# Optimization experiments

Measured on AMD Instinct MI355X. Metric: run time of the kernel, lower is better.

## Reference

```python
import jax, jax.numpy as jnp
import numpy as np

B, T = 32, 64
STOCH, DETER, HIDDEN = 1024, 4096, 1024
ACT_DIM, EMBED = 128, 1536
MIN_STD = 0.1
EPS = 1e-3  # dreamerv3-torch uses LayerNorm(eps=1e-3)


def _ln(x, g, b):
    m = jnp.mean(x, -1, keepdims=True)
    v = jnp.var(x, -1, keepdims=True)
    return (x - m) * jax.lax.rsqrt(v + EPS) * g + b


def setup_inputs() -> dict:
    key = jax.random.key(0)
    ks = jax.random.split(key, 24)

    def w(k, fan_in, fan_out):
        return jax.random.normal(k, (fan_in, fan_out), jnp.float32) / np.sqrt(fan_in)

    inp = {
        "embed": jax.random.normal(ks[0], (B, T, EMBED), jnp.float32),
        "action": jax.random.normal(ks[1], (B, T, ACT_DIM), jnp.float32),
        "is_first": jnp.zeros((B, T), jnp.bool_),
        "init_deter": jax.random.normal(ks[2], (B, DETER), jnp.float32),
        "init_stoch": jax.random.normal(ks[3], (B, STOCH), jnp.float32),
        "noise_prior": jax.random.normal(ks[4], (B, T, STOCH), jnp.float32),
        "noise_post": jax.random.normal(ks[5], (B, T, STOCH), jnp.float32),
        # _img_in_layers: Linear(stoch+act -> hidden, no bias) + LN + SiLU
        "W_in": w(ks[6], STOCH + ACT_DIM, HIDDEN),
        "g_in": 1.0 + 0.1 * jax.random.normal(ks[7], (HIDDEN,), jnp.float32),
        "b_in": 0.1 * jax.random.normal(ks[8], (HIDDEN,), jnp.float32),
        # GRUCell: Linear(hidden+deter -> 3*deter, no bias) + LN
        "W_gru": w(ks[9], HIDDEN + DETER, 3 * DETER),
        "g_gru": 1.0 + 0.1 * jax.random.normal(ks[10], (3 * DETER,), jnp.float32),
        "b_gru": 0.1 * jax.random.normal(ks[11], (3 * DETER,), jnp.float32),
        # _img_out_layers: Linear(deter -> hidden, no bias) + LN + SiLU
        "W_imgout": w(ks[12], DETER, HIDDEN),
        "g_io": 1.0 + 0.1 * jax.random.normal(ks[13], (HIDDEN,), jnp.float32),
        "b_io": 0.1 * jax.random.normal(ks[14], (HIDDEN,), jnp.float32),
        # _obs_out_layers: Linear(deter+embed -> hidden, no bias) + LN + SiLU
        "W_obsout": w(ks[15], DETER + EMBED, HIDDEN),
        "g_oo": 1.0 + 0.1 * jax.random.normal(ks[16], (HIDDEN,), jnp.float32),
        "b_oo": 0.1 * jax.random.normal(ks[17], (HIDDEN,), jnp.float32),
        # suff-stats layers: Linear(hidden -> 2*stoch) with bias
        "W_ims": w(ks[18], HIDDEN, 2 * STOCH),
        "b_ims": 0.01 * jax.random.normal(ks[19], (2 * STOCH,), jnp.float32),
        "W_obs": w(ks[20], HIDDEN, 2 * STOCH),
        "b_obs": 0.01 * jax.random.normal(ks[21], (2 * STOCH,), jnp.float32),
    }
    return inp


def _observe(embed, action, init_deter, init_stoch, noise_prior, noise_post,
             W_in, g_in, b_in, W_gru, g_gru, b_gru, W_imgout, g_io, b_io,
             W_obsout, g_oo, b_oo, W_ims, b_ims, W_obs, b_obs):
    def suff_stats(h, W, b, noise):
        stats = h @ W + b
        mean, std = jnp.split(stats, 2, -1)
        std = jax.nn.softplus(std) + MIN_STD  # std_act='softplus', mean_act='none'
        return mean, std, mean + std * noise

    def step(carry, xs):
        deter, stoch = carry
        e, a, n_p, n_q = xs
        # img_in: concat(prev_stoch, action) -> Linear -> LN -> SiLU
        x = jax.nn.silu(_ln(jnp.concatenate([stoch, a], -1) @ W_in, g_in, b_in))
        # GRUCell with layernorm (update_bias = -1)
        parts = _ln(jnp.concatenate([x, deter], -1) @ W_gru, g_gru, b_gru)
        reset, cand, update = jnp.split(parts, 3, -1)
        reset = jax.nn.sigmoid(reset)
        cand = jnp.tanh(reset * cand)
        update = jax.nn.sigmoid(update - 1.0)
        deter = update * cand + (1.0 - update) * deter
        # prior (imagination) suff stats + sample
        h_p = jax.nn.silu(_ln(deter @ W_imgout, g_io, b_io))
        mean_p, std_p, stoch_p = suff_stats(h_p, W_ims, b_ims, n_p)
        # posterior (observation) suff stats + sample
        h_q = jax.nn.silu(_ln(jnp.concatenate([deter, e], -1) @ W_obsout, g_oo, b_oo))
        mean_q, std_q, stoch_q = suff_stats(h_q, W_obs, b_obs, n_q)
        out = jnp.concatenate([deter, stoch_q, mean_q, std_q, stoch_p, mean_p, std_p], -1)
        return (deter, stoch_q), out

    xs = (jnp.swapaxes(embed, 0, 1), jnp.swapaxes(action, 0, 1),
          jnp.swapaxes(noise_prior, 0, 1), jnp.swapaxes(noise_post, 0, 1))
    _, outs = jax.lax.scan(step, (init_deter, init_stoch), xs)
    return jnp.swapaxes(outs, 0, 1)  # [B, T, deter + 6*stoch]


def reference(embed, action, is_first, init_deter, init_stoch, noise_prior, noise_post,
              W_in, g_in, b_in, W_gru, g_gru, b_gru, W_imgout, g_io, b_io,
              W_obsout, g_oo, b_oo, W_ims, b_ims, W_obs, b_obs):
    # is_first is all-False and state is given, so the init-mixing branch is never taken
    del is_first
    return _observe(embed, action, init_deter, init_stoch, noise_prior, noise_post,
                    W_in, g_in, b_in, W_gru, g_gru, b_gru, W_imgout, g_io, b_io,
                    W_obsout, g_oo, b_oo, W_ims, b_ims, W_obs, b_obs)
```

## Files before the change

### kernel.cpp

```cpp
#include <hip/hip_runtime.h>
#include <hip/hip_bf16.h>

#define T_ 64
#define DETER_ 4096
#define GRUN 12288

typedef __attribute__((ext_vector_type(8))) __bf16 bf16x8;
typedef __attribute__((ext_vector_type(4))) float f32x4;
typedef __attribute__((ext_vector_type(8))) unsigned short u16x8;
typedef __attribute__((ext_vector_type(4))) unsigned short u16x4;

__device__ inline unsigned short f2bf(float f) {
    union { float f; unsigned u; } x; x.f = f;
    unsigned r = x.u + 0x7fffu + ((x.u >> 16) & 1u);
    return (unsigned short)(r >> 16);
}
__device__ inline float sigmoidf_(float v) { return 1.f / (1.f + __expf(-v)); }
__device__ inline float siluf_(float v)    { return v / (1.f + __expf(-v)); }
__device__ inline float softplusf_(float v){ return fmaxf(v, 0.f) + __logf(1.f + __expf(-fabsf(v))); }
__device__ inline float tanhf_(float v)    { return 2.f / (1.f + __expf(-2.f * v)) - 1.f; }

__device__ inline void barrier_() {
    asm volatile("" ::: "memory");
    __builtin_amdgcn_s_barrier();
    asm volatile("" ::: "memory");
}
template <int N> __device__ inline void vmwaitN() {
    asm volatile("s_waitcnt vmcnt(%0)" :: "i"(N) : "memory");
}
__device__ inline void lgkmwait_() {
    asm volatile("s_waitcnt lgkmcnt(0)" ::: "memory");
}


__global__ __launch_bounds__(256) void k_pack(const float* __restrict__ W,
                                              unsigned short* __restrict__ dst,
                                              int K, int N) {
    long fid = (long)blockIdx.x * 256 + threadIdx.x;
    long nfr = (long)K * N / 8;
    if (fid >= nfr) return;
    int lane = (int)(fid & 63);
    long tile = fid >> 6;
    int ktiles = K >> 5;
    int k_t = (int)(tile % ktiles);
    int n_t = (int)(tile / ktiles);
    int c = lane & 15, kb = lane >> 4;
    int k0 = k_t * 32 + kb * 8;
    int n = n_t * 16 + c;
    unsigned short v[8];
#pragma unroll
    for (int i = 0; i < 8; i++) v[i] = f2bf(W[(long)(k0 + i) * N + n]);
    *reinterpret_cast<u16x8*>(dst + fid * 8) = *reinterpret_cast<u16x8*>(v);
}

__global__ __launch_bounds__(256) void k_conv(const float* __restrict__ s,
                                              unsigned short* __restrict__ d, long n) {
    long i = ((long)blockIdx.x * 256 + threadIdx.x) * 4;
    if (i >= n) return;
    f32x4 v = *reinterpret_cast<const f32x4*>(s + i);
    unsigned short o[4];
#pragma unroll
    for (int k = 0; k < 4; k++) o[k] = f2bf(v[k]);
    *reinterpret_cast<u16x4*>(d + i) = *reinterpret_cast<u16x4*>(o);
}

__global__ __launch_bounds__(256) void k_copy(const float* __restrict__ s,
                                              float* __restrict__ d, long n) {
    long i = ((long)blockIdx.x * 256 + threadIdx.x) * 4;
    if (i >= n) return;
    *reinterpret_cast<f32x4*>(d + i) = *reinterpret_cast<const f32x4*>(s + i);
}


template <int CW>
__device__ inline void stage_glds(unsigned short* chunk, const unsigned short* __restrict__ src,
                                  long ld, long k0) {
    constexpr int NI = (32 * CW * 2) / 4096;
    int wv = (int)threadIdx.x >> 6, lane = (int)threadIdx.x & 63;
#pragma unroll
    for (int i = 0; i < NI; ++i) {
        int obase = (wv * NI + i) << 10;
        int o = obase + lane * 16;
        int row = o / (CW * 2);
        int cb = o - row * (CW * 2);
        int gb = cb ^ ((row & 7) << 4);
        const char* ga = (const char*)(src + (long)row * ld + k0) + gb;
        __builtin_amdgcn_global_load_lds(
            (const __attribute__((address_space(1))) void*)ga,
            (__attribute__((address_space(3))) void*)(chunk + (obase >> 1)),
            16, 0, 0);
    }
}

__device__ inline void stage_ln512(unsigned short* chunk, const float* __restrict__ raw,
                                   int ld, int col0,
                                   const float* __restrict__ g, const float* __restrict__ b,
                                   const float* s_mean, const float* s_rstd) {
    int tid = threadIdx.x;
#pragma unroll
    for (int i = 0; i < 8; ++i) {
        int e = tid * 8 + i * 2048;
        int row = e >> 9, col = e & 511;
        float m = s_mean[row], rs = s_rstd[row];
        const float* sp = raw + (long)row * ld + col0 + col;
        unsigned short pk[8];
#pragma unroll
        for (int j = 0; j < 8; ++j) {
            float ln = (sp[j] - m) * rs * g[col0 + col + j] + b[col0 + col + j];
            pk[j] = f2bf(siluf_(ln));
        }
        int dcol = col ^ ((row & 7) << 3);
        *reinterpret_cast<u16x8*>(chunk + row * 512 + dcol) = *reinterpret_cast<u16x8*>(pk);
    }
}

__device__ inline void stage_ln256(unsigned short* chunk, const float* __restrict__ raw,
                                   int ld, int col0,
                                   const float* __restrict__ g, const float* __restrict__ b,
                                   const float* s_mean, const float* s_rstd) {
    int tid = threadIdx.x;
#pragma unroll
    for (int i = 0; i < 4; ++i) {
        int e = tid * 8 + i * 2048;
        int row = e >> 8, col = e & 255;
        float m = s_mean[row], rs = s_rstd[row];
        const float* sp = raw + (long)row * ld + col0 + col;
        unsigned short pk[8];
#pragma unroll
        for (int j = 0; j < 8; ++j) {
            float ln = (sp[j] - m) * rs * g[col0 + col + j] + b[col0 + col + j];
            pk[j] = f2bf(siluf_(ln));
        }
        int dcol = col ^ ((row & 7) << 3);
        *reinterpret_cast<u16x8*>(chunk + row * 256 + dcol) = *reinterpret_cast<u16x8*>(pk);
    }
}

__device__ inline void stage_lnsum(unsigned short* chunk, const float* __restrict__ hpart,
                                   const float* __restrict__ eprep, int t, int col0,
                                   const float* __restrict__ g, const float* __restrict__ b,
                                   const float* s_mean, const float* s_rstd) {
    int tid = threadIdx.x;
#pragma unroll
    for (int i = 0; i < 8; ++i) {
        int e = tid * 8 + i * 2048;
        int row = e >> 9, col = e & 511;
        int k = col0 + col;
        float m = s_mean[row], rs = s_rstd[row];
        const float* h0 = hpart + (long)row * 1024 + k;
        const float* ep = eprep + ((long)row * T_ + t) * 1024 + k;
        unsigned short pk[8];
#pragma unroll
        for (int jj = 0; jj < 8; jj += 4) {
            f32x4 v = *reinterpret_cast<const f32x4*>(h0 + jj);
            v += *reinterpret_cast<const f32x4*>(h0 + 32768 + jj);
            v += *reinterpret_cast<const f32x4*>(h0 + 65536 + jj);
            v += *reinterpret_cast<const f32x4*>(h0 + 98304 + jj);
            v += *reinterpret_cast<const f32x4*>(ep + jj);
#pragma unroll
            for (int j2 = 0; j2 < 4; ++j2) {
                float ln = (v[j2] - m) * rs * g[k + jj + j2] + b[k + jj + j2];
                pk[jj + j2] = f2bf(siluf_(ln));
            }
        }
        int dcol = col ^ ((row & 7) << 3);
        *reinterpret_cast<u16x8*>(chunk + row * 512 + dcol) = *reinterpret_cast<u16x8*>(pk);
    }
}

template <int CW>
__device__ inline void mfma_rh(const unsigned short* chunk, int row, int kb,
                               const unsigned short* __restrict__ bp, f32x4& acc) {
    constexpr int NKT = CW / 32;
    const unsigned short* ap = chunk + row * CW;
    int sw = (row & 7) << 3;
#pragma unroll
    for (int kt = 0; kt < NKT; ++kt) {
        bf16x8 a = *reinterpret_cast<const bf16x8*>(ap + ((kb * 8 + kt * 32) ^ sw));
        bf16x8 b = *reinterpret_cast<const bf16x8*>(bp + (long)kt * 512);
        acc = __builtin_amdgcn_mfma_f32_16x16x32_bf16(a, b, acc, 0, 0, 0);
    }
}

template <int CW>
__device__ inline void mfma2(const unsigned short* chunk, int c, int kb,
                             const unsigned short* __restrict__ bp,
                             f32x4& acc0, f32x4& acc1) {
    constexpr int NKT = CW / 32;
    const unsigned short* ap0 = chunk + c * CW;
    const unsigned short* ap1 = chunk + (16 + c) * CW;
    int sw = (c & 7) << 3;
#pragma unroll
    for (int kt = 0; kt < NKT; ++kt) {
        int off = (kb * 8 + kt * 32) ^ sw;
        bf16x8 b = *reinterpret_cast<const bf16x8*>(bp + (long)kt * 512);
        bf16x8 a0 = *reinterpret_cast<const bf16x8*>(ap0 + off);
        bf16x8 a1 = *reinterpret_cast<const bf16x8*>(ap1 + off);
        acc0 = __builtin_amdgcn_mfma_f32_16x16x32_bf16(a0, b, acc0, 0, 0, 0);
        acc1 = __builtin_amdgcn_mfma_f32_16x16x32_bf16(a1, b, acc1, 0, 0, 0);
    }
}

template <int CW, int NG, int NL>
__global__ __launch_bounds__(256) void k_gemm32(
    const unsigned short* __restrict__ Bp, int Ktiles, int ktg0,
    const unsigned short* __restrict__ srcA, long ldA,
    const float* __restrict__ lnraw, int lnld,
    const float* __restrict__ g_ln, const float* __restrict__ b_ln,
    const float* __restrict__ pstats, int nslab_in,
    const float* __restrict__ addin, long addin_ld,
    float* __restrict__ outp, long out_ld,
    float* __restrict__ partials, long prows)
{
    constexpr int NCH = NG + NL;
    constexpr int NI = (32 * CW * 2) / 4096;
    __shared__ __align__(16) unsigned short sb[2][32 * CW];
    __shared__ float s_out[32][34];
    __shared__ float s_mean[32], s_rstd[32];
    int tid = threadIdx.x;
    if (NL > 0) {
        if (tid < 32) {
            float s = 0.f, q = 0.f;
            for (int j = 0; j < nslab_in; ++j) {
                s += pstats[((long)j * 32 + tid) * 2];
                q += pstats[((long)j * 32 + tid) * 2 + 1];
            }
            float m = s * (1.f / 1024.f);
            s_mean[tid] = m;
            s_rstd[tid] = rsqrtf(q * (1.f / 1024.f) - m * m + 1e-3f);
        }
        __syncthreads();
    }
    int rowbase = blockIdx.y * 32;
    const unsigned short* srcAr = srcA + (long)rowbase * ldA;
    int lane = tid & 63, wv = tid >> 6;
    int nt = wv >> 1, rh = wv & 1;
    int c = lane & 15, kb = lane >> 4;
    int mrow = rh * 16 + c;
    long ntg = (long)blockIdx.x * 2 + nt;
    const unsigned short* bbase = Bp + (long)ntg * Ktiles * 512 + lane * 8;
    f32x4 acc = {0.f, 0.f, 0.f, 0.f};
    stage_glds<CW>(sb[0], srcAr, ldA, 0);
    for (int ch = 0; ch < NCH; ++ch) {
        int nx = ch + 1;
        if (nx < NG) stage_glds<CW>(sb[nx & 1], srcAr, ldA, (long)nx * CW);
        else if (nx < NCH) stage_ln512(sb[nx & 1], lnraw, lnld, (nx - NG) * 512,
                                       g_ln, b_ln, s_mean, s_rstd);
        if (ch < NG) { if (nx < NG) vmwaitN<NI>(); else vmwaitN<0>(); }
        if (nx >= NG && nx < NCH) lgkmwait_();
        barrier_();
        int kt0 = (ch < NG) ? (ktg0 + ch * (CW / 32)) : ((ch - NG) * 16);
        mfma_rh<CW>(sb[ch & 1], mrow, kb, bbase + (long)kt0 * 512, acc);
        barrier_();
    }
    __syncthreads();
#pragma unroll
    for (int j = 0; j < 4; ++j) s_out[rh * 16 + kb * 4 + j][nt * 16 + c] = acc[j];
    __syncthreads();
    int orow = tid >> 3, c4 = (tid & 7) * 4;
    long rg = rowbase + orow;
    float v[4]; float s = 0.f, q = 0.f;
#pragma unroll
    for (int i = 0; i < 4; ++i) {
        float x = s_out[orow][c4 + i];
        if (addin) x += addin[rg * addin_ld + blockIdx.x * 32 + c4 + i];
        v[i] = x; s += x; q += x * x;
    }
#pragma unroll
    for (int i = 0; i < 4; ++i) outp[rg * out_ld + blockIdx.x * 32 + c4 + i] = v[i];
    if (partials) {
#pragma unroll
        for (int m = 1; m < 8; m <<= 1) { s += __shfl_xor(s, m); q += __shfl_xor(q, m); }
        if ((tid & 7) == 0) {
            partials[((long)blockIdx.x * prows + rg) * 2] = s;
            partials[((long)blockIdx.x * prows + rg) * 2 + 1] = q;
        }
    }
}

__global__ __launch_bounds__(256, 3) void k_gru4(
    const unsigned short* __restrict__ Bp,
    const unsigned short* __restrict__ deterb,
    const float* __restrict__ x_raw, const float* __restrict__ px,
    const float* __restrict__ g_in, const float* __restrict__ b_in,
    float* __restrict__ Gp)
{
    __shared__ __align__(16) unsigned short sb[2][32 * 256];
    __shared__ float s_out[32][66];
    __shared__ float s_mean[32], s_rstd[32];
    int tid = threadIdx.x, lane = tid & 63, wv = tid >> 6;
    int c = lane & 15, kb = lane >> 4;
    int kq = blockIdx.y;
    long ntg = (long)blockIdx.x * 4 + wv;
    const unsigned short* bb = Bp + ntg * 160 * 512 + lane * 8;
    f32x4 acc0 = {0, 0, 0, 0}, acc1 = {0, 0, 0, 0};

    if (kq == 0) {
        if (tid < 32) {
            float s = 0.f, q = 0.f;
            for (int j = 0; j < 32; ++j) {
                s += px[((long)j * 32 + tid) * 2];
                q += px[((long)j * 32 + tid) * 2 + 1];
            }
            float m = s * (1.f / 1024.f);
            s_mean[tid] = m;
            s_rstd[tid] = rsqrtf(q * (1.f / 1024.f) - m * m + 1e-3f);
        }
        __syncthreads();
        stage_glds<256>(sb[0], deterb, 4096, 0);
        stage_ln256(sb[1], x_raw, 1024, 0, g_in, b_in, s_mean, s_rstd);
        vmwaitN<0>(); barrier_();
        mfma2<256>(sb[0], c, kb, bb + (long)32 * 512, acc0, acc1);
        barrier_();
        stage_ln256(sb[0], x_raw, 1024, 256, g_in, b_in, s_mean, s_rstd);
        lgkmwait_(); barrier_();
        mfma2<256>(sb[1], c, kb, bb, acc0, acc1);
        barrier_();
        stage_ln256(sb[1], x_raw, 1024, 512, g_in, b_in, s_mean, s_rstd);
        lgkmwait_(); barrier_();
        mfma2<256>(sb[0], c, kb, bb + (long)8 * 512, acc0, acc1);
        barrier_();
        stage_ln256(sb[0], x_raw, 1024, 768, g_in, b_in, s_mean, s_rstd);
        lgkmwait_(); barrier_();
        mfma2<256>(sb[1], c, kb, bb + (long)16 * 512, acc0, acc1);
        barrier_();
        mfma2<256>(sb[0], c, kb, bb + (long)24 * 512, acc0, acc1);
    } else {
        long o0 = 256 + (long)(kq - 1) * 1280;
        int kt0 = 40 + (kq - 1) * 40;
        stage_glds<256>(sb[0], deterb, 4096, o0);
        stage_glds<256>(sb[1], deterb, 4096, o0 + 256);
        for (int ch = 0; ch < 5; ++ch) {
            if (ch < 4) vmwaitN<4>(); else vmwaitN<0>();
            barrier_();
            mfma2<256>(sb[ch & 1], c, kb, bb + (long)(kt0 + 8 * ch) * 512, acc0, acc1);
            barrier_();
            if (ch + 2 < 5)
                stage_glds<256>(sb[ch & 1], deterb, 4096, o0 + 256 * (ch + 2));
        }
    }
    __syncthreads();
#pragma unroll
    for (int j = 0; j < 4; ++j) {
        s_out[kb * 4 + j][wv * 16 + c] = acc0[j];
        s_out[16 + kb * 4 + j][wv * 16 + c] = acc1[j];
    }
    __syncthreads();
    int row = tid >> 3, c8 = (tid & 7) * 8;
    float* G = Gp + (long)kq * 32 * GRUN + (long)row * GRUN + blockIdx.x * 64 + c8;
#pragma unroll
    for (int i = 0; i < 8; ++i) G[i] = s_out[row][c8 + i];
}

__global__ __launch_bounds__(1024) void k_deter4(
    const float* __restrict__ Gp,
    const float* __restrict__ g_gru, const float* __restrict__ b_gru,
    float* __restrict__ deterf, unsigned short* __restrict__ deterb,
    unsigned short* __restrict__ deter_allb, float* __restrict__ out, int t)
{
    __shared__ float gsh[GRUN];
    __shared__ float red[32];
    int r = blockIdx.x, tid = threadIdx.x;
    int lane = tid & 63, wv = tid >> 6;
    const float* g0 = Gp + (long)r * GRUN;
    float s = 0.f, q = 0.f;
#pragma unroll
    for (int i = 0; i < 3; ++i) {
        int col = (tid + i * 1024) * 4;
        f32x4 v = *reinterpret_cast<const f32x4*>(g0 + col);
        v += *reinterpret_cast<const f32x4*>(g0 + 393216 + col);
        v += *reinterpret_cast<const f32x4*>(g0 + 786432 + col);
        v += *reinterpret_cast<const f32x4*>(g0 + 1179648 + col);
        *reinterpret_cast<f32x4*>(gsh + col) = v;
#pragma unroll
        for (int j = 0; j < 4; ++j) { s += v[j]; q += v[j] * v[j]; }
    }
#pragma unroll
    for (int m = 1; m < 64; m <<= 1) { s += __shfl_xor(s, m); q += __shfl_xor(q, m); }
    if (lane == 0) { red[wv] = s; red[16 + wv] = q; }
    __syncthreads();
    float fs = 0.f, fq = 0.f;
#pragma unroll
    for (int i = 0; i < 16; ++i) { fs += red[i]; fq += red[16 + i]; }
    float mean = fs * (1.f / 12288.f);
    float rstd = rsqrtf(fq * (1.f / 12288.f) - mean * mean + 1e-3f);
    long orow = (long)r * T_ + t;
#pragma unroll
    for (int it = 0; it < 2; ++it) {
        int j = tid * 2 + it * 2048;
        float2 rr = *reinterpret_cast<const float2*>(gsh + j);
        float2 cc = *reinterpret_cast<const float2*>(gsh + 4096 + j);
        float2 uu = *reinterpret_cast<const float2*>(gsh + 8192 + j);
        float2 dd = *reinterpret_cast<const float2*>(deterf + (long)r * DETER_ + j);
        float dn[2]; unsigned short db[2];
#pragma unroll
        for (int i = 0; i < 2; ++i) {
            float gv = (i == 0) ? rr.x : rr.y;
            float cv = (i == 0) ? cc.x : cc.y;
            float uv = (i == 0) ? uu.x : uu.y;
            float dv = (i == 0) ? dd.x : dd.y;
            float lr = (gv - mean) * rstd * g_gru[j + i] + b_gru[j + i];
            float lc = (cv - mean) * rstd * g_gru[4096 + j + i] + b_gru[4096 + j + i];
            float lu = (uv - mean) * rstd * g_gru[8192 + j + i] + b_gru[8192 + j + i];
            float reset = sigmoidf_(lr);
            float cand = tanhf_(reset * lc);
            float upd = sigmoidf_(lu - 1.f);
            dn[i] = upd * cand + (1.f - upd) * dv;
            db[i] = f2bf(dn[i]);
        }
        float2 nd; nd.x = dn[0]; nd.y = dn[1];
        *reinterpret_cast<float2*>(deterf + (long)r * DETER_ + j) = nd;
        unsigned pk = (unsigned)db[0] | ((unsigned)db[1] << 16);
        *reinterpret_cast<unsigned*>(deterb + (long)r * DETER_ + j) = pk;
        *reinterpret_cast<unsigned*>(deter_allb + orow * DETER_ + j) = pk;
        *reinterpret_cast<float2*>(out + orow * 10240 + j) = nd;
    }
}

__global__ __launch_bounds__(256) void k_h4(
    const unsigned short* __restrict__ Wood,
    const unsigned short* __restrict__ deterb,
    float* __restrict__ hpart)
{
    __shared__ __align__(16) unsigned short sb[2][32 * 512];
    __shared__ float s_out[32][66];
    int tid = threadIdx.x, lane = tid & 63, wv = tid >> 6;
    int c = lane & 15, kb = lane >> 4;
    int n = blockIdx.x, kq = blockIdx.y;
    const unsigned short* bbase = Wood + ((long)(n * 4 + wv) * 128) * 512 + lane * 8;
    f32x4 acc0 = {0,0,0,0}, acc1 = {0,0,0,0};
    stage_glds<512>(sb[0], deterb, 4096, (long)kq * 1024);
    stage_glds<512>(sb[1], deterb, 4096, (long)kq * 1024 + 512);
    vmwaitN<8>(); barrier_();
    mfma2<512>(sb[0], c, kb, bbase + (long)(kq * 32) * 512, acc0, acc1);
    vmwaitN<0>(); barrier_();
    mfma2<512>(sb[1], c, kb, bbase + (long)(kq * 32 + 16) * 512, acc0, acc1);
    __syncthreads();
#pragma unroll
    for (int j = 0; j < 4; ++j) {
        s_out[kb * 4 + j][wv * 16 + c] = acc0[j];
        s_out[16 + kb * 4 + j][wv * 16 + c] = acc1[j];
    }
    __syncthreads();
    int row = tid >> 3, c8 = (tid & 7) * 8;
    float* hp = hpart + (long)kq * 32768 + (long)row * 1024 + n * 64 + c8;
#pragma unroll
    for (int i = 0; i < 8; ++i) hp[i] = s_out[row][c8 + i];
}

__global__ __launch_bounds__(256) void k_statsq2(
    const unsigned short* __restrict__ Bp, const float* __restrict__ hpart,
    const float* __restrict__ E_pre,
    const float* __restrict__ g_oo, const float* __restrict__ b_oo,
    const float* __restrict__ bias,
    const float* __restrict__ noise, float* __restrict__ out,
    unsigned short* __restrict__ stochb, int t)
{
    __shared__ __align__(16) unsigned short sb[2][32 * 512];
    __shared__ float s_out[32][66];
    __shared__ float s_mean[32], s_rstd[32];
    int tid = threadIdx.x, lane = tid & 63, wv = tid >> 6;
    int c = lane & 15, kb = lane >> 4;
    {
        int row = tid >> 3, c0 = (tid & 7) * 128;
        const float* h0 = hpart + (long)row * 1024 + c0;
        const float* ep = E_pre + ((long)row * T_ + t) * 1024 + c0;
        float s = 0.f, q = 0.f;
#pragma unroll 8
        for (int kk = 0; kk < 128; kk += 4) {
            f32x4 v = *reinterpret_cast<const f32x4*>(h0 + kk);
            v += *reinterpret_cast<const f32x4*>(h0 + 32768 + kk);
            v += *reinterpret_cast<const f32x4*>(h0 + 65536 + kk);
            v += *reinterpret_cast<const f32x4*>(h0 + 98304 + kk);
            v += *reinterpret_cast<const f32x4*>(ep + kk);
#pragma unroll
            for (int j2 = 0; j2 < 4; ++j2) { s += v[j2]; q += v[j2] * v[j2]; }
        }
#pragma unroll
        for (int m = 1; m < 8; m <<= 1) { s += __shfl_xor(s, m); q += __shfl_xor(q, m); }
        if ((tid & 7) == 0) {
            float mm = s * (1.f / 1024.f);
            s_mean[row] = mm;
            s_rstd[row] = rsqrtf(q * (1.f / 1024.f) - mm * mm + 1e-3f);
        }
    }
    __syncthreads();
    int part = wv >> 1, nt = wv & 1;
    long ntg = (long)part * 64 + blockIdx.x * 2 + nt;
    const unsigned short* bbase = Bp + ntg * 32 * 512 + lane * 8;
    f32x4 acc0 = {0,0,0,0}, acc1 = {0,0,0,0};
    stage_lnsum(sb[0], hpart, E_pre, t, 0, g_oo, b_oo, s_mean, s_rstd);
    stage_lnsum(sb[1], hpart, E_pre, t, 512, g_oo, b_oo, s_mean, s_rstd);
    lgkmwait_(); barrier_();
    mfma2<512>(sb[0], c, kb, bbase, acc0, acc1);
    mfma2<512>(sb[1], c, kb, bbase + 16 * 512, acc0, acc1);
    __syncthreads();
    float bv = bias[ntg * 16 + c];
#pragma unroll
    for (int j = 0; j < 4; ++j) {
        s_out[kb * 4 + j][part * 32 + nt * 16 + c] = acc0[j] + bv;
        s_out[16 + kb * 4 + j][part * 32 + nt * 16 + c] = acc1[j] + bv;
    }
    __syncthreads();
    int r = tid >> 3, j0 = (tid & 7) * 4;
    long orow = (long)r * T_ + t;
#pragma unroll
    for (int i = 0; i < 4; ++i) {
        int j = j0 + i;
        float mean = s_out[r][j];
        float sd = softplusf_(s_out[r][32 + j]) + 0.1f;
        int cg2 = blockIdx.x * 32 + j;
        float st = mean + sd * noise[orow * 1024 + cg2];
        float* op = out + orow * 10240;
        op[4096 + cg2] = st; op[5120 + cg2] = mean; op[6144 + cg2] = sd;
        stochb[(long)r * 1024 + cg2] = f2bf(st);
    }
}

__global__ __launch_bounds__(256) void k_bstats(
    const unsigned short* __restrict__ Bp, const unsigned short* __restrict__ h_pb,
    const float* __restrict__ bias, const float* __restrict__ noise,
    float* __restrict__ out)
{
    __shared__ __align__(16) unsigned short sb[2][32 * 512];
    __shared__ float s_out[32][66];
    int tid = threadIdx.x;
    int lane = tid & 63, wv = tid >> 6;
    int part = wv >> 1, nt = wv & 1;
    int c = lane & 15, kb = lane >> 4;
    int s_ = blockIdx.x, rowbase = blockIdx.y * 32;
    const unsigned short* A = h_pb + (long)rowbase * 1024;
    long ntg = (long)part * 64 + s_ * 2 + nt;
    const unsigned short* bbase = Bp + ntg * 32 * 512 + lane * 8;
    f32x4 acc0 = {0.f,0.f,0.f,0.f}, acc1 = {0.f,0.f,0.f,0.f};
    stage_glds<512>(sb[0], A, 1024, 0);
    stage_glds<512>(sb[1], A, 1024, 512);
    vmwaitN<8>(); barrier_();
    mfma_rh<512>(sb[0], c, kb, bbase, acc0);
    mfma_rh<512>(sb[0], 16 + c, kb, bbase, acc1);
    vmwaitN<0>(); barrier_();
    mfma_rh<512>(sb[1], c, kb, bbase + 16 * 512, acc0);
    mfma_rh<512>(sb[1], 16 + c, kb, bbase + 16 * 512, acc1);
    __syncthreads();
    float bv = bias[ntg * 16 + c];
#pragma unroll
    for (int j = 0; j < 4; ++j) {
        s_out[kb * 4 + j][part * 32 + nt * 16 + c] = acc0[j] + bv;
        s_out[16 + kb * 4 + j][part * 32 + nt * 16 + c] = acc1[j] + bv;
    }
    __syncthreads();
    int r = tid >> 3, j0 = (tid & 7) * 4;
    long orow = rowbase + r;
#pragma unroll
    for (int i = 0; i < 4; ++i) {
        int j = j0 + i;
        float mean = s_out[r][j];
        float sd = softplusf_(s_out[r][32 + j]) + 0.1f;
        int cg2 = s_ * 32 + j;
        float st = mean + sd * noise[orow * 1024 + cg2];
        float* op = out + orow * 10240;
        op[7168 + cg2] = st; op[8192 + cg2] = mean; op[9216 + cg2] = sd;
    }
}

__global__ __launch_bounds__(256) void k_bfin(const float* __restrict__ hp_raw,
                                              const float* __restrict__ pbh,
                                              const float* __restrict__ g_io,
                                              const float* __restrict__ b_io,
                                              unsigned short* __restrict__ h_pb) {
    int row = blockIdx.x * 8 + ((int)threadIdx.x >> 5);
    int l = threadIdx.x & 31;
    float s = pbh[((long)l * 2048 + row) * 2];
    float q = pbh[((long)l * 2048 + row) * 2 + 1];
#pragma unroll
    for (int m = 16; m; m >>= 1) { s += __shfl_xor(s, m, 32); q += __shfl_xor(q, m, 32); }
    float mn = s * (1.f / 1024.f);
    float rs = rsqrtf(q * (1.f / 1024.f) - mn * mn + 1e-3f);
#pragma unroll
    for (int i = 0; i < 8; ++i) {
        int col = i * 128 + l * 4;
        f32x4 v = *reinterpret_cast<const f32x4*>(hp_raw + (long)row * 1024 + col);
        unsigned short pk[4];
#pragma unroll
        for (int j = 0; j < 4; ++j) {
            float ln = (v[j] - mn) * rs * g_io[col + j] + b_io[col + j];
            pk[j] = f2bf(siluf_(ln));
        }
        *reinterpret_cast<u16x4*>(h_pb + (long)row * 1024 + col) = *reinterpret_cast<u16x4*>(pk);
    }
}


extern "C" void kernel_launch(void* const* d_in, const int* in_sizes, int n_in,
                              void* d_out, int out_size, void* d_ws, size_t ws_size,
                              hipStream_t stream) {
    const float* embed      = (const float*)d_in[0];
    const float* action     = (const float*)d_in[1];
    const float* init_deter = (const float*)d_in[3];
    const float* init_stoch = (const float*)d_in[4];
    const float* noise_pr   = (const float*)d_in[5];
    const float* noise_po   = (const float*)d_in[6];
    const float* W_in       = (const float*)d_in[7];
    const float* g_in       = (const float*)d_in[8];
    const float* b_in       = (const float*)d_in[9];
    const float* W_gru      = (const float*)d_in[10];
    const float* g_gru      = (const float*)d_in[11];
    const float* b_gru      = (const float*)d_in[12];
    const float* W_io       = (const float*)d_in[13];
    const float* g_io       = (const float*)d_in[14];
    const float* b_io       = (const float*)d_in[15];
    const float* W_oo       = (const float*)d_in[16];
    const float* g_oo       = (const float*)d_in[17];
    const float* b_oo       = (const float*)d_in[18];
    const float* W_ims      = (const float*)d_in[19];
    const float* b_ims      = (const float*)d_in[20];
    const float* W_obs      = (const float*)d_in[21];
    const float* b_obs      = (const float*)d_in[22];
    float* out = (float*)d_out;

    char* ws = (char*)d_ws;
    size_t off = 0;
    auto alloc = [&](size_t bytes) {
        size_t r = off;
        off = (off + bytes + 255) & ~(size_t)255;
        return r;
    };
    unsigned short* pWgru  = (unsigned short*)(ws + alloc((size_t)5120 * 12288 * 2));
    unsigned short* pWin_s = (unsigned short*)(ws + alloc((size_t)1024 * 1024 * 2));
    unsigned short* pWin_a = (unsigned short*)(ws + alloc((size_t)128 * 1024 * 2));
    unsigned short* pWio   = (unsigned short*)(ws + alloc((size_t)4096 * 1024 * 2));
    unsigned short* pWood  = (unsigned short*)(ws + alloc((size_t)4096 * 1024 * 2));
    unsigned short* pWooe  = (unsigned short*)(ws + alloc((size_t)1536 * 1024 * 2));
    unsigned short* pWims  = (unsigned short*)(ws + alloc((size_t)1024 * 2048 * 2));
    unsigned short* pWobs  = (unsigned short*)(ws + alloc((size_t)1024 * 2048 * 2));
    unsigned short* act_bf = (unsigned short*)(ws + alloc((size_t)2048 * 128 * 2));
    unsigned short* emb_bf = (unsigned short*)(ws + alloc((size_t)2048 * 1536 * 2));
    float* A_pre  = (float*)(ws + alloc((size_t)2048 * 1024 * 4));
    float* E_pre  = (float*)(ws + alloc((size_t)2048 * 1024 * 4));
    float* x_raw  = (float*)(ws + alloc((size_t)32 * 1024 * 4));
    float* Gp     = (float*)(ws + alloc((size_t)4 * 32 * GRUN * 4));
    float* deterf = (float*)(ws + alloc((size_t)32 * DETER_ * 4));
    unsigned short* deterb     = (unsigned short*)(ws + alloc((size_t)32 * DETER_ * 2));
    unsigned short* deter_allb = (unsigned short*)(ws + alloc((size_t)2048 * DETER_ * 2));
    unsigned short* stochb = (unsigned short*)(ws + alloc((size_t)32 * 1024 * 2));
    float* hp_raw = (float*)(ws + alloc((size_t)2048 * 1024 * 4));
    unsigned short* h_pb = (unsigned short*)(ws + alloc((size_t)2048 * 1024 * 2));
    float* px  = (float*)(ws + alloc((size_t)32 * 32 * 2 * 4));
    float* pbh = (float*)(ws + alloc((size_t)32 * 2048 * 2 * 4));
    float* hpart = (float*)(ws + alloc((size_t)4 * 32 * 1024 * 4));
    (void)ws_size; (void)out_size; (void)n_in; (void)in_sizes;

    auto packgrid = [](long K, long N) { return (unsigned)((K * N / 8 + 255) / 256); };

    k_pack<<<packgrid(5120, 12288), 256, 0, stream>>>(W_gru, pWgru, 5120, 12288);
    k_pack<<<packgrid(1024, 1024), 256, 0, stream>>>(W_in, pWin_s, 1024, 1024);
    k_pack<<<packgrid(128, 1024), 256, 0, stream>>>(W_in + (size_t)1024 * 1024, pWin_a, 128, 1024);
    k_pack<<<packgrid(4096, 1024), 256, 0, stream>>>(W_io, pWio, 4096, 1024);
    k_pack<<<packgrid(4096, 1024), 256, 0, stream>>>(W_oo, pWood, 4096, 1024);
    k_pack<<<packgrid(1536, 1024), 256, 0, stream>>>(W_oo + (size_t)4096 * 1024, pWooe, 1536, 1024);
    k_pack<<<packgrid(1024, 2048), 256, 0, stream>>>(W_ims, pWims, 1024, 2048);
    k_pack<<<packgrid(1024, 2048), 256, 0, stream>>>(W_obs, pWobs, 1024, 2048);
    k_conv<<<(2048 * 128 / 4 + 255) / 256, 256, 0, stream>>>(action, act_bf, 2048L * 128);
    k_conv<<<(2048 * 1536 / 4 + 255) / 256, 256, 0, stream>>>(embed, emb_bf, 2048L * 1536);
    k_conv<<<(32 * 1024 / 4 + 255) / 256, 256, 0, stream>>>(init_stoch, stochb, 32L * 1024);
    k_conv<<<(32 * 4096 / 4 + 255) / 256, 256, 0, stream>>>(init_deter, deterb, 32L * 4096);
    k_copy<<<(32 * 4096 / 4 + 255) / 256, 256, 0, stream>>>(init_deter, deterf, 32L * 4096);
    k_gemm32<128, 1, 0><<<dim3(32, 64), 256, 0, stream>>>(
        pWin_a, 4, 0, act_bf, 128, nullptr, 0, nullptr, nullptr, nullptr, 0,
        nullptr, 0, A_pre, 1024, nullptr, 0);
    k_gemm32<512, 3, 0><<<dim3(32, 64), 256, 0, stream>>>(
        pWooe, 48, 0, emb_bf, 1536, nullptr, 0, nullptr, nullptr, nullptr, 0,
        nullptr, 0, E_pre, 1024, nullptr, 0);

    for (int t = 0; t < T_; ++t) {
        k_gemm32<512, 2, 0><<<dim3(32, 1), 256, 0, stream>>>(
            pWin_s, 32, 0, stochb, 1024, nullptr, 0, nullptr, nullptr, nullptr, 0,
            A_pre + (size_t)t * 1024, (long)T_ * 1024, x_raw, 1024, px, 32);
        k_gru4<<<dim3(192, 4), 256, 0, stream>>>(pWgru, deterb, x_raw, px, g_in, b_in, Gp);
        k_deter4<<<32, 1024, 0, stream>>>(Gp, g_gru, b_gru, deterf, deterb,
                                          deter_allb, out, t);
        k_h4<<<dim3(16, 4), 256, 0, stream>>>(pWood, deterb, hpart);
        k_statsq2<<<32, 256, 0, stream>>>(pWobs, hpart, E_pre, g_oo, b_oo, b_obs,
                                          noise_po, out, stochb, t);
    }

    k_gemm32<512, 8, 0><<<dim3(32, 64), 256, 0, stream>>>(
        pWio, 128, 0, deter_allb, 4096, nullptr, 0, nullptr, nullptr, nullptr, 0,
        nullptr, 0, hp_raw, 1024, pbh, 2048);
    k_bfin<<<256, 256, 0, stream>>>(hp_raw, pbh, g_io, b_io, h_pb);
    k_bstats<<<dim3(32, 64), 256, 0, stream>>>(pWims, h_pb, b_ims, noise_pr, out);
}
```

Baseline: 6.041 ms.

## Fuse per-step recurrent kernels into two cooperative kernels with grid syncs

Replaces the five per-timestep launches with two cooperative kernels. The first fuses the stoch-input GEMM with the GRU GEMM and emits partial LayerNorm stats. The second fuses the GRU gate update, the h GEMM and the posterior stats, using grid.sync between phases. This aims to cut launch overhead and inter-kernel gaps in the serial 64-step loop. It relies on cooperative launch succeeding with 768 blocks, which needs enough co-resident occupancy. Grid-wide barriers add their own cost, and the fused deter phase now runs on 128 smaller blocks instead of 32 blocks of 1024 threads.

```diff
diff --git a/kernel.cpp b/kernel.cpp
--- a/kernel.cpp
+++ b/kernel.cpp
@@ -1,5 +1,8 @@
 #include <hip/hip_runtime.h>
 #include <hip/hip_bf16.h>
+#include <hip/hip_cooperative_groups.h>
+
+namespace cg = cooperative_groups;
 
 #define T_ 64
 #define DETER_ 4096
@@ -278,27 +281,73 @@
     }
 }
 
-__global__ __launch_bounds__(256, 3) void k_gru4(
-    const unsigned short* __restrict__ Bp,
+__global__ __launch_bounds__(256, 3) void k_xgru(
+    const unsigned short* __restrict__ pWin_s,
+    const unsigned short* __restrict__ pWgru,
+    const unsigned short* __restrict__ stochb,
     const unsigned short* __restrict__ deterb,
-    const float* __restrict__ x_raw, const float* __restrict__ px,
+    const float* __restrict__ A_pre,
+    float* __restrict__ x_raw, float* __restrict__ px,
     const float* __restrict__ g_in, const float* __restrict__ b_in,
-    float* __restrict__ Gp)
+    float* __restrict__ Gp, float* __restrict__ pg, int t)
 {
     __shared__ __align__(16) unsigned short sb[2][32 * 256];
     __shared__ float s_out[32][66];
     __shared__ float s_mean[32], s_rstd[32];
-    int tid = threadIdx.x, lane = tid & 63, wv = tid >> 6;
+    cg::grid_group grid = cg::this_grid();
+    int bid = blockIdx.x, tid = threadIdx.x;
+    int lane = tid & 63, wv = tid >> 6;
     int c = lane & 15, kb = lane >> 4;
-    int kq = blockIdx.y;
-    long ntg = (long)blockIdx.x * 4 + wv;
-    const unsigned short* bb = Bp + ntg * 160 * 512 + lane * 8;
+
+    if (bid < 16) {
+        long ntg = (long)bid * 4 + wv;
+        const unsigned short* bb = pWin_s + ntg * 32 * 512 + lane * 8;
+        f32x4 a0 = {0, 0, 0, 0}, a1 = {0, 0, 0, 0};
+        stage_glds<256>(sb[0], stochb, 1024, 0);
+        stage_glds<256>(sb[1], stochb, 1024, 256);
+#pragma unroll
+        for (int ch = 0; ch < 4; ++ch) {
+            if (ch < 3) vmwaitN<4>(); else vmwaitN<0>();
+            barrier_();
+            mfma2<256>(sb[ch & 1], c, kb, bb + (long)(8 * ch) * 512, a0, a1);
+            barrier_();
+            if (ch < 2) stage_glds<256>(sb[ch & 1], stochb, 1024, (long)(ch + 2) * 256);
+        }
+        __syncthreads();
+#pragma unroll
+        for (int j = 0; j < 4; ++j) {
+            s_out[kb * 4 + j][wv * 16 + c] = a0[j];
+            s_out[16 + kb * 4 + j][wv * 16 + c] = a1[j];
+        }
+        __syncthreads();
+        int row = tid >> 3, c8 = (tid & 7) * 8;
+        const float* ap = A_pre + ((long)row * T_ + t) * 1024 + bid * 64 + c8;
+        float s = 0.f, q = 0.f, v[8];
+#pragma unroll
+        for (int i = 0; i < 8; ++i) {
+            float x = s_out[row][c8 + i] + ap[i];
+            v[i] = x; s += x; q += x * x;
+        }
+#pragma unroll
+        for (int i = 0; i < 8; ++i) x_raw[(long)row * 1024 + bid * 64 + c8 + i] = v[i];
+#pragma unroll
+        for (int m = 1; m < 8; m <<= 1) { s += __shfl_xor(s, m); q += __shfl_xor(q, m); }
+        if ((tid & 7) == 0) {
+            px[((long)bid * 32 + row) * 2] = s;
+            px[((long)bid * 32 + row) * 2 + 1] = q;
+        }
+    }
+    grid.sync();
+
+    int gb = bid % 192, kq = bid / 192;
+    long ntg = (long)gb * 4 + wv;
+    const unsigned short* bb = pWgru + ntg * 160 * 512 + lane * 8;
     f32x4 acc0 = {0, 0, 0, 0}, acc1 = {0, 0, 0, 0};
 
     if (kq == 0) {
         if (tid < 32) {
             float s = 0.f, q = 0.f;
-            for (int j = 0; j < 32; ++j) {
+            for (int j = 0; j < 16; ++j) {
                 s += px[((long)j * 32 + tid) * 2];
                 q += px[((long)j * 32 + tid) * 2 + 1];
             }
@@ -347,6 +396,244 @@
     }
     __syncthreads();
     int row = tid >> 3, c8 = (tid & 7) * 8;
+    float* G = Gp + (long)kq * 32 * GRUN + (long)row * GRUN + gb * 64 + c8;
+    float s = 0.f, q = 0.f;
+#pragma unroll
+    for (int i = 0; i < 8; ++i) {
+        float x = s_out[row][c8 + i];
+        G[i] = x; s += x; q += x * x;
+    }
+#pragma unroll
+    for (int m = 1; m < 8; m <<= 1) { s += __shfl_xor(s, m); q += __shfl_xor(q, m); }
+    if ((tid & 7) == 0) {
+        long slab = (long)kq * 192 + gb;
+        pg[(slab * 32 + row) * 2] = s;
+        pg[(slab * 32 + row) * 2 + 1] = q;
+    }
+}
+
+__global__ __launch_bounds__(256, 2) void k_dhs(
+    const float* __restrict__ Gp, const float* __restrict__ pg,
+    const float* __restrict__ g_gru, const float* __restrict__ b_gru,
+    float* __restrict__ deterf, unsigned short* __restrict__ deterb,
+    unsigned short* __restrict__ deter_allb,
+    const unsigned short* __restrict__ pWood, float* __restrict__ hpart,
+    const unsigned short* __restrict__ pWobs, const float* __restrict__ E_pre,
+    const float* __restrict__ g_oo, const float* __restrict__ b_oo,
+    const float* __restrict__ b_obs, const float* __restrict__ noise_po,
+    float* __restrict__ out, unsigned short* __restrict__ stochb, int t)
+{
+    __shared__ __align__(16) unsigned short sb[2][32 * 512];
+    __shared__ float s_out[32][66];
+    __shared__ float s_mean[32], s_rstd[32];
+    __shared__ float red[8];
+    cg::grid_group grid = cg::this_grid();
+    int bid = blockIdx.x, tid = threadIdx.x;
+    int lane = tid & 63, wv = tid >> 6;
+    int c = lane & 15, kb = lane >> 4;
+
+    {
+        int r = bid >> 2, cq = bid & 3;
+        float s = 0.f, q = 0.f;
+        for (int sl = tid; sl < 768; sl += 256) {
+            s += pg[((long)sl * 32 + r) * 2];
+            q += pg[((long)sl * 32 + r) * 2 + 1];
+        }
+#pragma unroll
+        for (int m = 1; m < 64; m <<= 1) { s += __shfl_xor(s, m); q += __shfl_xor(q, m); }
+        if (lane == 0) { red[wv] = s; red[4 + wv] = q; }
+        __syncthreads();
+        float fs = red[0] + red[1] + red[2] + red[3];
+        float fq = red[4] + red[5] + red[6] + red[7];
+        float mean = fs * (1.f / 12288.f);
+        float rstd = rsqrtf(fq * (1.f / 12288.f) - mean * mean + 1e-3f);
+        int j = cq * 1024 + tid * 4;
+        const float* g0 = Gp + (long)r * GRUN;
+        f32x4 rr = *reinterpret_cast<const f32x4*>(g0 + j);
+        rr += *reinterpret_cast<const f32x4*>(g0 + 393216 + j);
+        rr += *reinterpret_cast<const f32x4*>(g0 + 786432 + j);
+        rr += *reinterpret_cast<const f32x4*>(g0 + 1179648 + j);
+        f32x4 cc = *reinterpret_cast<const f32x4*>(g0 + 4096 + j);
+        cc += *reinterpret_cast<const f32x4*>(g0 + 393216 + 4096 + j);
+        cc += *reinterpret_cast<const f32x4*>(g0 + 786432 + 4096 + j);
+        cc += *reinterpret_cast<const f32x4*>(g0 + 1179648 + 4096 + j);
+        f32x4 uu = *reinterpret_cast<const f32x4*>(g0 + 8192 + j);
+        uu += *reinterpret_cast<const f32x4*>(g0 + 393216 + 8192 + j);
+        uu += *reinterpret_cast<const f32x4*>(g0 + 786432 + 8192 + j);
+        uu += *reinterpret_cast<const f32x4*>(g0 + 1179648 + 8192 + j);
+        f32x4 dd = *reinterpret_cast<const f32x4*>(deterf + (long)r * DETER_ + j);
+        f32x4 nd; unsigned short db[4];
+#pragma unroll
+        for (int i = 0; i < 4; ++i) {
+            float lr = (rr[i] - mean) * rstd * g_gru[j + i] + b_gru[j + i];
+            float lc = (cc[i] - mean) * rstd * g_gru[4096 + j + i] + b_gru[4096 + j + i];
+            float lu = (uu[i] - mean) * rstd * g_gru[8192 + j + i] + b_gru[8192 + j + i];
+            float reset = sigmoidf_(lr);
+            float cand = tanhf_(reset * lc);
+            float upd = sigmoidf_(lu - 1.f);
+            nd[i] = upd * cand + (1.f - upd) * dd[i];
+            db[i] = f2bf(nd[i]);
+        }
+        long orow = (long)r * T_ + t;
+        *reinterpret_cast<f32x4*>(deterf + (long)r * DETER_ + j) = nd;
+        *reinterpret_cast<u16x4*>(deterb + (long)r * DETER_ + j) = *reinterpret_cast<u16x4*>(db);
+        *reinterpret_cast<u16x4*>(deter_allb + orow * DETER_ + j) = *reinterpret_cast<u16x4*>(db);
+        *reinterpret_cast<f32x4*>(out + orow * 10240 + j) = nd;
+    }
+    grid.sync();
+
+    if (bid < 64) {
+        int n = bid & 15, kq = bid >> 4;
+        const unsigned short* bbase = pWood + ((long)(n * 4 + wv) * 128) * 512 + lane * 8;
+        f32x4 acc0 = {0,0,0,0}, acc1 = {0,0,0,0};
+        stage_glds<512>(sb[0], deterb, 4096, (long)kq * 1024);
+        stage_glds<512>(sb[1], deterb, 4096, (long)kq * 1024 + 512);
+        vmwaitN<8>(); barrier_();
+        mfma2<512>(sb[0], c, kb, bbase + (long)(kq * 32) * 512, acc0, acc1);
+        vmwaitN<0>(); barrier_();
+        mfma2<512>(sb[1], c, kb, bbase + (long)(kq * 32 + 16) * 512, acc0, acc1);
+        __syncthreads();
+#pragma unroll
+        for (int jj = 0; jj < 4; ++jj) {
+            s_out[kb * 4 + jj][wv * 16 + c] = acc0[jj];
+            s_out[16 + kb * 4 + jj][wv * 16 + c] = acc1[jj];
+        }
+        __syncthreads();
+        int row = tid >> 3, c8 = (tid & 7) * 8;
+        float* hp = hpart + (long)kq * 32768 + (long)row * 1024 + n * 64 + c8;
+#pragma unroll
+        for (int i = 0; i < 8; ++i) hp[i] = s_out[row][c8 + i];
+    }
+    grid.sync();
+
+    if (bid < 32) {
+        {
+            int row = tid >> 3, c0 = (tid & 7) * 128;
+            const float* h0 = hpart + (long)row * 1024 + c0;
+            const float* ep = E_pre + ((long)row * T_ + t) * 1024 + c0;
+            float s = 0.f, q = 0.f;
+#pragma unroll 8
+            for (int kk = 0; kk < 128; kk += 4) {
+                f32x4 v = *reinterpret_cast<const f32x4*>(h0 + kk);
+                v += *reinterpret_cast<const f32x4*>(h0 + 32768 + kk);
+                v += *reinterpret_cast<const f32x4*>(h0 + 65536 + kk);
+                v += *reinterpret_cast<const f32x4*>(h0 + 98304 + kk);
+                v += *reinterpret_cast<const f32x4*>(ep + kk);
+#pragma unroll
+                for (int j2 = 0; j2 < 4; ++j2) { s += v[j2]; q += v[j2] * v[j2]; }
+            }
+#pragma unroll
+            for (int m = 1; m < 8; m <<= 1) { s += __shfl_xor(s, m); q += __shfl_xor(q, m); }
+            if ((tid & 7) == 0) {
+                float mm = s * (1.f / 1024.f);
+                s_mean[row] = mm;
+                s_rstd[row] = rsqrtf(q * (1.f / 1024.f) - mm * mm + 1e-3f);
+            }
+        }
+        __syncthreads();
+        int part = wv >> 1, nt = wv & 1;
+        long ntg = (long)part * 64 + bid * 2 + nt;
+        const unsigned short* bbase = pWobs + ntg * 32 * 512 + lane * 8;
+        f32x4 acc0 = {0,0,0,0}, acc1 = {0,0,0,0};
+        stage_lnsum(sb[0], hpart, E_pre, t, 0, g_oo, b_oo, s_mean, s_rstd);
+        stage_lnsum(sb[1], hpart, E_pre, t, 512, g_oo, b_oo, s_mean, s_rstd);
+        lgkmwait_(); barrier_();
+        mfma2<512>(sb[0], c, kb, bbase, acc0, acc1);
+        mfma2<512>(sb[1], c, kb, bbase + 16 * 512, acc0, acc1);
+        __syncthreads();
+        float bv = b_obs[ntg * 16 + c];
+#pragma unroll
+        for (int jj = 0; jj < 4; ++jj) {
+            s_out[kb * 4 + jj][part * 32 + nt * 16 + c] = acc0[jj] + bv;
+            s_out[16 + kb * 4 + jj][part * 32 + nt * 16 + c] = acc1[jj] + bv;
+        }
+        __syncthreads();
+        int r = tid >> 3, j0 = (tid & 7) * 4;
+        long orow = (long)r * T_ + t;
+#pragma unroll
+        for (int i = 0; i < 4; ++i) {
+            int jj = j0 + i;
+            float mean = s_out[r][jj];
+            float sd = softplusf_(s_out[r][32 + jj]) + 0.1f;
+            int cg2 = bid * 32 + jj;
+            float st = mean + sd * noise_po[orow * 1024 + cg2];
+            float* op = out + orow * 10240;
+            op[4096 + cg2] = st; op[5120 + cg2] = mean; op[6144 + cg2] = sd;
+            stochb[(long)r * 1024 + cg2] = f2bf(st);
+        }
+    }
+}
+
+
+__global__ __launch_bounds__(256, 3) void k_gru4(
+    const unsigned short* __restrict__ Bp,
+    const unsigned short* __restrict__ deterb,
+    const float* __restrict__ x_raw, const float* __restrict__ px,
+    const float* __restrict__ g_in, const float* __restrict__ b_in,
+    float* __restrict__ Gp)
+{
+    __shared__ __align__(16) unsigned short sb[2][32 * 256];
+    __shared__ float s_out[32][66];
+    __shared__ float s_mean[32], s_rstd[32];
+    int tid = threadIdx.x, lane = tid & 63, wv = tid >> 6;
+    int c = lane & 15, kb = lane >> 4;
+    int kq = blockIdx.y;
+    long ntg = (long)blockIdx.x * 4 + wv;
+    const unsigned short* bb = Bp + ntg * 160 * 512 + lane * 8;
+    f32x4 acc0 = {0, 0, 0, 0}, acc1 = {0, 0, 0, 0};
+
+    if (kq == 0) {
+        if (tid < 32) {
+            float s = 0.f, q = 0.f;
+            for (int j = 0; j < 32; ++j) {
+                s += px[((long)j * 32 + tid) * 2];
+                q += px[((long)j * 32 + tid) * 2 + 1];
+            }
+            float m = s * (1.f / 1024.f);
+            s_mean[tid] = m;
+            s_rstd[tid] = rsqrtf(q * (1.f / 1024.f) - m * m + 1e-3f);
+        }
+        __syncthreads();
+        stage_glds<256>(sb[0], deterb, 4096, 0);
+        stage_ln256(sb[1], x_raw, 1024, 0, g_in, b_in, s_mean, s_rstd);
+        vmwaitN<0>(); barrier_();
+        mfma2<256>(sb[0], c, kb, bb + (long)32 * 512, acc0, acc1);
+        barrier_();
+        stage_ln256(sb[0], x_raw, 1024, 256, g_in, b_in, s_mean, s_rstd);
+        lgkmwait_(); barrier_();
+        mfma2<256>(sb[1], c, kb, bb, acc0, acc1);
+        barrier_();
+        stage_ln256(sb[1], x_raw, 1024, 512, g_in, b_in, s_mean, s_rstd);
+        lgkmwait_(); barrier_();
+        mfma2<256>(sb[0], c, kb, bb + (long)8 * 512, acc0, acc1);
+        barrier_();
+        stage_ln256(sb[0], x_raw, 1024, 768, g_in, b_in, s_mean, s_rstd);
+        lgkmwait_(); barrier_();
+        mfma2<256>(sb[1], c, kb, bb + (long)16 * 512, acc0, acc1);
+        barrier_();
+        mfma2<256>(sb[0], c, kb, bb + (long)24 * 512, acc0, acc1);
+    } else {
+        long o0 = 256 + (long)(kq - 1) * 1280;
+        int kt0 = 40 + (kq - 1) * 40;
+        stage_glds<256>(sb[0], deterb, 4096, o0);
+        stage_glds<256>(sb[1], deterb, 4096, o0 + 256);
+        for (int ch = 0; ch < 5; ++ch) {
+            if (ch < 4) vmwaitN<4>(); else vmwaitN<0>();
+            barrier_();
+            mfma2<256>(sb[ch & 1], c, kb, bb + (long)(kt0 + 8 * ch) * 512, acc0, acc1);
+            barrier_();
+            if (ch + 2 < 5)
+                stage_glds<256>(sb[ch & 1], deterb, 4096, o0 + 256 * (ch + 2));
+        }
+    }
+    __syncthreads();
+#pragma unroll
+    for (int j = 0; j < 4; ++j) {
+        s_out[kb * 4 + j][wv * 16 + c] = acc0[j];
+        s_out[16 + kb * 4 + j][wv * 16 + c] = acc1[j];
+    }
+    __syncthreads();
+    int row = tid >> 3, c8 = (tid & 7) * 8;
     float* G = Gp + (long)kq * 32 * GRUN + (long)row * GRUN + blockIdx.x * 64 + c8;
 #pragma unroll
     for (int i = 0; i < 8; ++i) G[i] = s_out[row][c8 + i];
@@ -646,6 +933,7 @@
     float* hp_raw = (float*)(ws + alloc((size_t)2048 * 1024 * 4));
     unsigned short* h_pb = (unsigned short*)(ws + alloc((size_t)2048 * 1024 * 2));
     float* px  = (float*)(ws + alloc((size_t)32 * 32 * 2 * 4));
+    float* pg  = (float*)(ws + alloc((size_t)768 * 32 * 2 * 4));
     float* pbh = (float*)(ws + alloc((size_t)32 * 2048 * 2 * 4));
     float* hpart = (float*)(ws + alloc((size_t)4 * 32 * 1024 * 4));
     (void)ws_size; (void)out_size; (void)n_in; (void)in_sizes;
@@ -672,16 +960,57 @@
         pWooe, 48, 0, emb_bf, 1536, nullptr, 0, nullptr, nullptr, nullptr, 0,
         nullptr, 0, E_pre, 1024, nullptr, 0);
 
-    for (int t = 0; t < T_; ++t) {
-        k_gemm32<512, 2, 0><<<dim3(32, 1), 256, 0, stream>>>(
-            pWin_s, 32, 0, stochb, 1024, nullptr, 0, nullptr, nullptr, nullptr, 0,
-            A_pre + (size_t)t * 1024, (long)T_ * 1024, x_raw, 1024, px, 32);
-        k_gru4<<<dim3(192, 4), 256, 0, stream>>>(pWgru, deterb, x_raw, px, g_in, b_in, Gp);
-        k_deter4<<<32, 1024, 0, stream>>>(Gp, g_gru, b_gru, deterf, deterb,
-                                          deter_allb, out, t);
-        k_h4<<<dim3(16, 4), 256, 0, stream>>>(pWood, deterb, hpart);
-        k_statsq2<<<32, 256, 0, stream>>>(pWobs, hpart, E_pre, g_oo, b_oo, b_obs,
-                                          noise_po, out, stochb, t);
+    bool coop_ok = true;
+    {
+        void* a1[] = { (void*)&pWin_s, (void*)&pWgru, (void*)&stochb, (void*)&deterb,
+                       (void*)&A_pre, (void*)&x_raw, (void*)&px, (void*)&g_in, (void*)&b_in,
+                       (void*)&Gp, (void*)&pg, nullptr };
+        int t0 = 0;
+        a1[11] = (void*)&t0;
+        hipError_t rc = hipLaunchCooperativeKernel((const void*)k_xgru, dim3(768), dim3(256),
+                                                   a1, 0, stream);
+        if (rc != hipSuccess) { (void)hipGetLastError(); coop_ok = false; }
+        else {
+            void* a2[] = { (void*)&Gp, (void*)&pg, (void*)&g_gru, (void*)&b_gru,
+                           (void*)&deterf, (void*)&deterb, (void*)&deter_allb,
+                           (void*)&pWood, (void*)&hpart, (void*)&pWobs, (void*)&E_pre,
+                           (void*)&g_oo, (void*)&b_oo, (void*)&b_obs, (void*)&noise_po,
+                           (void*)&out, (void*)&stochb, (void*)&t0 };
+            rc = hipLaunchCooperativeKernel((const void*)k_dhs, dim3(128), dim3(256),
+                                            a2, 0, stream);
+            if (rc != hipSuccess) { (void)hipGetLastError(); coop_ok = false; }
+        }
+    }
+
+    if (coop_ok) {
+        static int ts[T_];
+        for (int t = 1; t < T_; ++t) {
+            ts[t] = t;
+            void* a1[] = { (void*)&pWin_s, (void*)&pWgru, (void*)&stochb, (void*)&deterb,
+                           (void*)&A_pre, (void*)&x_raw, (void*)&px, (void*)&g_in, (void*)&b_in,
+                           (void*)&Gp, (void*)&pg, (void*)&ts[t] };
+            (void)hipLaunchCooperativeKernel((const void*)k_xgru, dim3(768), dim3(256),
+                                             a1, 0, stream);
+            void* a2[] = { (void*)&Gp, (void*)&pg, (void*)&g_gru, (void*)&b_gru,
+                           (void*)&deterf, (void*)&deterb, (void*)&deter_allb,
+                           (void*)&pWood, (void*)&hpart, (void*)&pWobs, (void*)&E_pre,
+                           (void*)&g_oo, (void*)&b_oo, (void*)&b_obs, (void*)&noise_po,
+                           (void*)&out, (void*)&stochb, (void*)&ts[t] };
+            (void)hipLaunchCooperativeKernel((const void*)k_dhs, dim3(128), dim3(256),
+                                             a2, 0, stream);
+        }
+    } else {
+        for (int t = 0; t < T_; ++t) {
+            k_gemm32<512, 2, 0><<<dim3(32, 1), 256, 0, stream>>>(
+                pWin_s, 32, 0, stochb, 1024, nullptr, 0, nullptr, nullptr, nullptr, 0,
+                A_pre + (size_t)t * 1024, (long)T_ * 1024, x_raw, 1024, px, 32);
+            k_gru4<<<dim3(192, 4), 256, 0, stream>>>(pWgru, deterb, x_raw, px, g_in, b_in, Gp);
+            k_deter4<<<32, 1024, 0, stream>>>(Gp, g_gru, b_gru, deterf, deterb,
+                                              deter_allb, out, t);
+            k_h4<<<dim3(16, 4), 256, 0, stream>>>(pWood, deterb, hpart);
+            k_statsq2<<<32, 256, 0, stream>>>(pWobs, hpart, E_pre, g_oo, b_oo, b_obs,
+                                              noise_po, out, stochb, t);
+        }
     }
 
     k_gemm32<512, 8, 0><<<dim3(32, 64), 256, 0, stream>>>(
```

Result: slower. 14.30 ms (+136.6%).
